# Performance work log

Measured on AMD Instinct MI355X. Metric: run time of the kernel, lower is better.

## Reference

```python
import jax, jax.numpy as jnp
import numpy as np

B, F, T, E, H = 32, 512, 2000, 256, 128
EPS = 1e-7


def setup_inputs() -> dict:
    key = jax.random.key(0)
    ks = jax.random.split(key, 12)
    s = 0.05
    return {
        "y1": jax.random.normal(ks[0], (B, F, T), jnp.float32),
        "in_state2": jnp.zeros((2, B, H, 2), jnp.float32),
        "enc_w": jax.random.normal(ks[1], (E, F), jnp.float32) * s,   # conv1x1 weight
        "gamma": jnp.ones((E,), jnp.float32),
        "beta": jnp.zeros((E,), jnp.float32),
        "Wih1": jax.random.normal(ks[2], (4 * H, E), jnp.float32) * s,
        "Whh1": jax.random.normal(ks[3], (4 * H, H), jnp.float32) * s,
        "bih1": jax.random.normal(ks[4], (4 * H,), jnp.float32) * s,
        "bhh1": jax.random.normal(ks[5], (4 * H,), jnp.float32) * s,
        "Wih2": jax.random.normal(ks[6], (4 * H, H), jnp.float32) * s,
        "Whh2": jax.random.normal(ks[7], (4 * H, H), jnp.float32) * s,
        "bih2": jax.random.normal(ks[8], (4 * H,), jnp.float32) * s,
        "bhh2": jax.random.normal(ks[9], (4 * H,), jnp.float32) * s,
        "Wd": jax.random.normal(ks[10], (E, H), jnp.float32) * s,    # dense: H -> E
        "bd": jnp.zeros((E,), jnp.float32),
        "dec_w": jax.random.normal(ks[11], (F, E), jnp.float32) * s, # conv1x1 weight
    }


def _lstm_scan(x_tbd, h0, c0, Wih, Whh, b):
    # x_tbd: [T, B, D]; torch gate order i, f, g, o
    def step(carry, xt):
        h, c = carry
        z = xt @ Wih.T + h @ Whh.T + b
        i, f, g, o = jnp.split(z, 4, axis=-1)
        c = jax.nn.sigmoid(f) * c + jax.nn.sigmoid(i) * jnp.tanh(g)
        h = jax.nn.sigmoid(o) * jnp.tanh(c)
        return (h, c), h
    (hT, cT), ys = jax.lax.scan(step, (h0, c0), x_tbd)
    return ys, hT, cT


def reference(y1, in_state2, enc_w, gamma, beta, Wih1, Whh1, bih1, bhh1,
              Wih2, Whh2, bih2, bhh2, Wd, bd, dec_w):
    # encoder conv1x1: [B, F, T] -> [B, T, E]
    enc = jnp.einsum('ef,bft->bte', enc_w, y1)
    # instant (channel-wise) layer norm over E
    mean = jnp.mean(enc, axis=-1, keepdims=True)
    var = jnp.mean(jnp.square(enc - mean), axis=-1, keepdims=True)
    normed = (enc - mean) / jnp.sqrt(var + EPS) * gamma + beta
    # separation block (dropout is identity in eval mode)
    h1, c1 = in_state2[0, :, :, 0], in_state2[0, :, :, 1]
    h2, c2 = in_state2[1, :, :, 0], in_state2[1, :, :, 1]
    x_tbd = jnp.transpose(normed, (1, 0, 2))          # [T, B, E]
    ys1, h1o, c1o = _lstm_scan(x_tbd, h1, c1, Wih1, Whh1, bih1 + bhh1)
    ys2, h2o, c2o = _lstm_scan(ys1, h2, c2, Wih2, Whh2, bih2 + bhh2)
    x2 = jnp.transpose(ys2, (1, 0, 2))                # [B, T, H]
    mask = jax.nn.sigmoid(x2 @ Wd.T + bd)             # [B, T, E]
    estimated = mask * enc                            # [B, T, E]
    decoded = jnp.einsum('fe,bte->bft', dec_w, estimated)  # [B, F, T]
    h = jnp.stack([h1o, h2o], axis=0)                 # [2, B, H]
    c = jnp.stack([c1o, c2o], axis=0)
    out_state = jnp.stack([h, c], axis=-1)            # [2, B, H, 2]
    return decoded, out_state
```

## Files before the change

kernel.cpp:

```cpp
#include <hip/hip_runtime.h>

typedef __bf16 bf16;
typedef __bf16 bf16x8 __attribute__((ext_vector_type(8)));
typedef float f32x4 __attribute__((ext_vector_type(4)));

#define MFMA16(a, b, c) __builtin_amdgcn_mfma_f32_16x16x32_bf16((a), (b), (c), 0, 0, 0)

static constexpr int Bn = 32, Fn = 512, Tn = 2000, En = 256, Hn = 128, G4 = 512;
static constexpr long DECN = 32768000;

__device__ __forceinline__ float sigm(float x) {
  float e = __builtin_amdgcn_exp2f(x * -1.442695040888963f);
  return __builtin_amdgcn_rcpf(1.0f + e);
}
__device__ __forceinline__ float tanh_(float x) {
  float e = __builtin_amdgcn_exp2f(x * 2.885390081777926f);
  return 1.0f - 2.0f * __builtin_amdgcn_rcpf(e + 1.0f);
}
__device__ __forceinline__ float b2f(ushort u) {
  union { float f; unsigned v; } x; x.v = ((unsigned)u) << 16; return x.f;
}
__device__ __forceinline__ ushort f2b(float f) {
  return __builtin_bit_cast(ushort, (bf16)f);
}

__global__ void k_detect(const unsigned* __restrict__ gamma_raw, int* __restrict__ flag) {
  if (threadIdx.x == 0) *flag = (gamma_raw[0] == 0x3F803F80u) ? 0 : 1;
}

struct CvtArgs {
  const void* src[15];
  long n[15];
  long off[15];
};
__global__ void k_cvt_all(CvtArgs args, bf16* __restrict__ prm,
                          const int* __restrict__ flag) {
  int seg = blockIdx.y;
  long n = args.n[seg];
  bf16* dst = prm + args.off[seg];
  long i = blockIdx.x * (long)blockDim.x + threadIdx.x;
  long stride = (long)gridDim.x * blockDim.x;
  if (*flag) {
    const float* s = (const float*)args.src[seg];
    for (; i < n; i += stride) dst[i] = (bf16)s[i];
  } else {
    const bf16* s = (const bf16*)args.src[seg];
    for (; i < n; i += stride) dst[i] = s[i];
  }
}

__global__ void k_transpose(const void* __restrict__ y1, bf16* __restrict__ y1T,
                            const int* __restrict__ flag) {
  __shared__ ushort tile[32][34];
  int tx = threadIdx.x, ty = threadIdx.y;
  int b = blockIdx.z, f0 = blockIdx.y * 32, t0 = blockIdx.x * 32;
  int isf32 = *flag;
  ushort* dst = (ushort*)y1T;
#pragma unroll
  for (int j = 0; j < 4; ++j) {
    int fl = ty + 8 * j, t = t0 + tx;
    if (t < Tn) {
      long idx = ((long)b * Fn + f0 + fl) * Tn + t;
      tile[fl][tx] = isf32 ? f2b(((const float*)y1)[idx]) : ((const ushort*)y1)[idx];
    }
  }
  __syncthreads();
#pragma unroll
  for (int j = 0; j < 4; ++j) {
    int tl = ty + 8 * j, t = t0 + tl;
    if (t < Tn) dst[((long)b * Tn + t) * Fn + f0 + tx] = tile[tx][tl];
  }
}

__global__ __launch_bounds__(256) void k_enc_ln(
    const bf16* __restrict__ y1T, const bf16* __restrict__ enc_w,
    bf16* __restrict__ enc_b, float2* __restrict__ stats) {
  __shared__ float zl[16][257];
  int tid = threadIdx.x;
  int wv = tid >> 6, lane = tid & 63, q = lane >> 4, l16 = lane & 15;
  long bt0 = (long)blockIdx.x * 16;
  f32x4 acc[4] = {};
  const bf16* Arow = y1T + (bt0 + l16) * Fn;
  for (int kt = 0; kt < 16; ++kt) {
    bf16x8 a = *(const bf16x8*)(Arow + kt * 32 + q * 8);
#pragma unroll
    for (int i = 0; i < 4; ++i) {
      int nt = wv * 4 + i;
      bf16x8 bfr = *(const bf16x8*)(enc_w + (nt * 16 + l16) * Fn + kt * 32 + q * 8);
      acc[i] = MFMA16(a, bfr, acc[i]);
    }
  }
#pragma unroll
  for (int i = 0; i < 4; ++i) {
    int col = (wv * 4 + i) * 16 + l16;
#pragma unroll
    for (int r = 0; r < 4; ++r) zl[q * 4 + r][col] = acc[i][r];
  }
  __syncthreads();
  {
    int row = tid >> 4, ii = tid & 15;
    float s = 0.f, ss = 0.f;
#pragma unroll
    for (int j = 0; j < 16; ++j) { float v = zl[row][ii + 16 * j]; s += v; ss += v * v; }
#pragma unroll
    for (int m = 1; m < 16; m <<= 1) { s += __shfl_xor(s, m, 64); ss += __shfl_xor(ss, m, 64); }
    if (ii == 0) {
      float mean = s * (1.0f / 256.0f);
      float var = ss * (1.0f / 256.0f) - mean * mean;
      stats[bt0 + row] = make_float2(mean, rsqrtf(var + 1e-7f));
    }
  }
#pragma unroll
  for (int r = 0; r < 16; ++r)
    enc_b[(bt0 + r) * En + tid] = (bf16)zl[r][tid];
}

__global__ __launch_bounds__(256) void k_pre1(
    const bf16* __restrict__ enc_b, const float2* __restrict__ stats,
    const bf16* __restrict__ gamma, const bf16* __restrict__ beta,
    const bf16* __restrict__ Wih1, const bf16* __restrict__ bih1,
    const bf16* __restrict__ bhh1, bf16* __restrict__ pre1r) {
  int tid = threadIdx.x, wv = tid >> 6, lane = tid & 63, q = lane >> 4, l16 = lane & 15;
  int t = blockIdx.x >> 1, wh = blockIdx.x & 1;
  int b = wh * 16 + l16;
  long row = (long)b * Tn + t;
  float2 st = stats[row];
  const bf16* Arow = enc_b + row * En;
  f32x4 acc[8] = {};
  float bsum[8];
#pragma unroll
  for (int i = 0; i < 8; ++i) {
    int nt = wv * 8 + i;
    int orig = (nt & 3) * 128 + (nt >> 2) * 16 + l16;
    bsum[i] = (float)bih1[orig] + (float)bhh1[orig];
  }
  for (int kt = 0; kt < 8; ++kt) {
    bf16x8 a = *(const bf16x8*)(Arow + kt * 32 + q * 8);
    bf16x8 g8 = *(const bf16x8*)(gamma + kt * 32 + q * 8);
    bf16x8 e8 = *(const bf16x8*)(beta + kt * 32 + q * 8);
    bf16x8 x;
#pragma unroll
    for (int j = 0; j < 8; ++j) {
      float rg = st.y * (float)g8[j];
      x[j] = (bf16)((float)a[j] * rg + ((float)e8[j] - st.x * rg));
    }
#pragma unroll
    for (int i = 0; i < 8; ++i) {
      int nt = wv * 8 + i;
      int orig = (nt & 3) * 128 + (nt >> 2) * 16 + l16;
      bf16x8 bfr = *(const bf16x8*)(Wih1 + orig * En + kt * 32 + q * 8);
      acc[i] = MFMA16(x, bfr, acc[i]);
    }
  }
  ushort* dst = (ushort*)pre1r;
#pragma unroll
  for (int hg = 0; hg < 2; ++hg) {
    int hid = (wv * 2 + hg) * 16 + l16;
#pragma unroll
    for (int r = 0; r < 4; ++r) {
      int B = wh * 16 + q * 4 + r;
      ushort4 pk;
      pk.x = f2b(acc[hg * 4 + 0][r] + bsum[hg * 4 + 0]);
      pk.y = f2b(acc[hg * 4 + 1][r] + bsum[hg * 4 + 1]);
      pk.z = f2b(acc[hg * 4 + 2][r] + bsum[hg * 4 + 2]);
      pk.w = f2b(acc[hg * 4 + 3][r] + bsum[hg * 4 + 3]);
      *(ushort4*)(dst + (((long)t * Bn + B) * Hn + hid) * 4) = pk;
    }
  }
}

__global__ __launch_bounds__(512, 2) void k_rec(
    const bf16* __restrict__ pre1r, const bf16* __restrict__ state_c,
    const bf16* __restrict__ Whh1, const bf16* __restrict__ Wih2,
    const bf16* __restrict__ Whh2, const bf16* __restrict__ bih2,
    const bf16* __restrict__ bhh2, bf16* __restrict__ ys2,
    void* __restrict__ out_base, const int* __restrict__ flag) {
  __shared__ __align__(16) bf16 h1buf[2][16 * 136];
  __shared__ __align__(16) bf16 h2buf[2][16 * 136];

  int tid = threadIdx.x, wv = tid >> 6, lane = tid & 63, q = lane >> 4, l16 = lane & 15;
  int b0 = blockIdx.x * 4;
  int isf32 = *flag;
  int hid = wv * 16 + l16;
  int brow = b0 + q;
  int pos = q * 4;

  bf16x8 W1[4][4], Wx[4][4], Wh[4][4];
  float b2s[4];
#pragma unroll
  for (int g = 0; g < 4; ++g) {
    int n = g * 128 + hid;
#pragma unroll
    for (int kt = 0; kt < 4; ++kt) {
      W1[g][kt] = *(const bf16x8*)(Whh1 + n * Hn + kt * 32 + q * 8);
      Wx[g][kt] = *(const bf16x8*)(Wih2 + n * Hn + kt * 32 + q * 8);
      Wh[g][kt] = *(const bf16x8*)(Whh2 + n * Hn + kt * 32 + q * 8);
    }
    b2s[g] = (float)bih2[n] + (float)bhh2[n];
  }
#pragma unroll
  for (int g = 0; g < 4; ++g)
#pragma unroll
    for (int kt = 0; kt < 4; ++kt) {
      f32x4 t1 = __builtin_bit_cast(f32x4, W1[g][kt]);
      f32x4 t2 = __builtin_bit_cast(f32x4, Wx[g][kt]);
      f32x4 t3 = __builtin_bit_cast(f32x4, Wh[g][kt]);
      asm volatile("" : "+v"(t1), "+v"(t2), "+v"(t3));
      W1[g][kt] = __builtin_bit_cast(bf16x8, t1);
      Wx[g][kt] = __builtin_bit_cast(bf16x8, t2);
      Wh[g][kt] = __builtin_bit_cast(bf16x8, t3);
    }

  for (int i = tid; i < 16 * 136; i += 512) {
    h1buf[0][i] = (bf16)0.f; h1buf[1][i] = (bf16)0.f;
    h2buf[0][i] = (bf16)0.f; h2buf[1][i] = (bf16)0.f;
  }
  __syncthreads();

  float c1, c2;
  {
    long i1 = ((long)(0 * Bn + brow) * Hn + hid) * 2;
    long i2 = ((long)(1 * Bn + brow) * Hn + hid) * 2;
    h1buf[1][pos * 136 + hid] = state_c[i1];
    h2buf[1][pos * 136 + hid] = state_c[i2];
    c1 = (float)state_c[i1 + 1];
    c2 = (float)state_c[i2 + 1];
  }
  ushort4 pz = *(const ushort4*)((const ushort*)pre1r + ((long)brow * Hn + hid) * 4);
  __syncthreads();

  for (int t = 0; t < Tn; ++t) {
    int cur = t & 1, prv = cur ^ 1;
    f32x4 acc[4];
#pragma unroll
    for (int g = 0; g < 4; ++g) { f32x4 z = {}; acc[g] = z; }
    acc[0][0] = b2f(pz.x); acc[1][0] = b2f(pz.y);
    acc[2][0] = b2f(pz.z); acc[3][0] = b2f(pz.w);
    {
      int tn = (t + 1 < Tn) ? t + 1 : t;
      pz = *(const ushort4*)((const ushort*)pre1r +
                             (((long)tn * Bn + brow) * Hn + hid) * 4);
    }
#pragma unroll
    for (int kt = 0; kt < 4; ++kt) {
      bf16x8 a = *(const bf16x8*)(&h1buf[prv][l16 * 136 + kt * 32 + q * 8]);
#pragma unroll
      for (int g = 0; g < 4; ++g) acc[g] = MFMA16(a, W1[g][kt], acc[g]);
    }
    {
      float ig = sigm(acc[0][0]), fg = sigm(acc[1][0]);
      float gg = tanh_(acc[2][0]), og = sigm(acc[3][0]);
      c1 = fg * c1 + ig * gg;
      float h = og * tanh_(c1);
      h1buf[cur][pos * 136 + hid] = (bf16)h;
      if (t == Tn - 1) {
        long o = DECN + ((long)(0 * Bn + brow) * Hn + hid) * 2;
        if (isf32) { ((float*)out_base)[o] = h; ((float*)out_base)[o + 1] = c1; }
        else { ((bf16*)out_base)[o] = (bf16)h; ((bf16*)out_base)[o + 1] = (bf16)c1; }
      }
    }
    __syncthreads();
#pragma unroll
    for (int g = 0; g < 4; ++g) { f32x4 z = {}; acc[g] = z; acc[g][0] = b2s[g]; }
#pragma unroll
    for (int kt = 0; kt < 4; ++kt) {
      bf16x8 ax = *(const bf16x8*)(&h1buf[cur][l16 * 136 + kt * 32 + q * 8]);
      bf16x8 ah = *(const bf16x8*)(&h2buf[prv][l16 * 136 + kt * 32 + q * 8]);
#pragma unroll
      for (int g = 0; g < 4; ++g) {
        acc[g] = MFMA16(ax, Wx[g][kt], acc[g]);
        acc[g] = MFMA16(ah, Wh[g][kt], acc[g]);
      }
    }
    {
      float ig = sigm(acc[0][0]), fg = sigm(acc[1][0]);
      float gg = tanh_(acc[2][0]), og = sigm(acc[3][0]);
      c2 = fg * c2 + ig * gg;
      float h = og * tanh_(c2);
      h2buf[cur][pos * 136 + hid] = (bf16)h;
      ys2[((long)brow * Tn + t) * Hn + hid] = (bf16)h;
      if (t == Tn - 1) {
        long o = DECN + ((long)(1 * Bn + brow) * Hn + hid) * 2;
        if (isf32) { ((float*)out_base)[o] = h; ((float*)out_base)[o + 1] = c2; }
        else { ((bf16*)out_base)[o] = (bf16)h; ((bf16*)out_base)[o + 1] = (bf16)c2; }
      }
    }
    __syncthreads();
  }
}

__global__ __launch_bounds__(256) void k_mask(
    const bf16* __restrict__ ys2, const bf16* __restrict__ Wd,
    const bf16* __restrict__ bd, bf16* __restrict__ enc_est) {
  int tid = threadIdx.x, wv = tid >> 6, lane = tid & 63, q = lane >> 4, l16 = lane & 15;
  long bt0 = (long)blockIdx.x * 16;
  f32x4 acc[4] = {};
  const bf16* Arow = ys2 + (bt0 + l16) * Hn;
  for (int kt = 0; kt < 4; ++kt) {
    bf16x8 a = *(const bf16x8*)(Arow + kt * 32 + q * 8);
#pragma unroll
    for (int i = 0; i < 4; ++i) {
      int nt = wv * 4 + i;
      bf16x8 bfr = *(const bf16x8*)(Wd + (nt * 16 + l16) * Hn + kt * 32 + q * 8);
      acc[i] = MFMA16(a, bfr, acc[i]);
    }
  }
#pragma unroll
  for (int i = 0; i < 4; ++i) {
    int col = (wv * 4 + i) * 16 + l16;
    float bdv = (float)bd[col];
#pragma unroll
    for (int r = 0; r < 4; ++r) {
      int row = q * 4 + r;
      float m = sigm(acc[i][r] + bdv);
      long idx = (bt0 + row) * En + col;
      enc_est[idx] = (bf16)(m * (float)enc_est[idx]);
    }
  }
}

__global__ __launch_bounds__(256) void k_dec(
    const bf16* __restrict__ est_b, const bf16* __restrict__ dec_w,
    void* __restrict__ outp, const int* __restrict__ flag) {
  int tid = threadIdx.x, wv = tid >> 6, lane = tid & 63, q = lane >> 4, l16 = lane & 15;
  long bt0 = (long)blockIdx.x * 16;
  int b = (int)(bt0 / Tn), t0 = (int)(bt0 % Tn);
  int isf32 = *flag;
  f32x4 acc[8] = {};
  const bf16* Arow = est_b + (bt0 + l16) * En;
  for (int kt = 0; kt < 8; ++kt) {
    bf16x8 a = *(const bf16x8*)(Arow + kt * 32 + q * 8);
#pragma unroll
    for (int i = 0; i < 8; ++i) {
      int nt = wv * 8 + i;
      bf16x8 bfr = *(const bf16x8*)(dec_w + (nt * 16 + l16) * En + kt * 32 + q * 8);
      acc[i] = MFMA16(a, bfr, acc[i]);
    }
  }
#pragma unroll
  for (int i = 0; i < 8; ++i) {
    int f = (wv * 8 + i) * 16 + l16;
    long off = ((long)b * Fn + f) * Tn + t0 + q * 4;
    if (isf32) {
      *(float4*)((float*)outp + off) =
          make_float4(acc[i][0], acc[i][1], acc[i][2], acc[i][3]);
    } else {
      ushort4 pk;
      pk.x = f2b(acc[i][0]);
      pk.y = f2b(acc[i][1]);
      pk.z = f2b(acc[i][2]);
      pk.w = f2b(acc[i][3]);
      *(ushort4*)((ushort*)outp + off) = pk;
    }
  }
}

extern "C" void kernel_launch(void* const* d_in, const int* in_sizes, int n_in,
                              void* d_out, int out_size, void* d_ws, size_t ws_size,
                              hipStream_t stream) {
  (void)in_sizes; (void)n_in; (void)out_size; (void)ws_size;

  char* ws = (char*)d_ws;
  bf16*   enc_b = (bf16*)(ws);
  float2* stats = (float2*)(ws + 32768000);
  bf16*   ys2   = (bf16*)(ws + 33280000);
  bf16*   prm   = (bf16*)(ws + 49664000);
  int*    flag  = (int*)(ws + 50947584);

  static const long pn[15] = {131072, 256, 256, 131072, 65536, 512, 512,
                              65536, 65536, 512, 512, 32768, 256, 131072, 16384};
  static const int  src_idx[15] = {2, 3, 4, 5, 6, 7, 8, 9, 10, 11, 12, 13, 14, 15, 1};
  long poff[15]; long o = 0;
  for (int i = 0; i < 15; ++i) { poff[i] = o; o += pn[i]; }
  bf16* enc_w = prm + poff[0];
  bf16* gamma = prm + poff[1];
  bf16* beta  = prm + poff[2];
  bf16* Wih1  = prm + poff[3];
  bf16* Whh1  = prm + poff[4];
  bf16* bih1  = prm + poff[5];
  bf16* bhh1  = prm + poff[6];
  bf16* Wih2  = prm + poff[7];
  bf16* Whh2  = prm + poff[8];
  bf16* bih2  = prm + poff[9];
  bf16* bhh2  = prm + poff[10];
  bf16* Wd    = prm + poff[11];
  bf16* bd    = prm + poff[12];
  bf16* dec_w = prm + poff[13];
  bf16* state_c = prm + poff[14];

  bf16* y1T   = (bf16*)d_out;
  bf16* pre1r = (bf16*)d_out;

  k_detect<<<1, 64, 0, stream>>>((const unsigned*)d_in[3], flag);
  CvtArgs ca;
  for (int i = 0; i < 15; ++i) {
    ca.src[i] = d_in[src_idx[i]];
    ca.n[i] = pn[i];
    ca.off[i] = poff[i];
  }
  k_cvt_all<<<dim3(512, 15, 1), 256, 0, stream>>>(ca, prm, flag);
  k_transpose<<<dim3(63, 16, 32), dim3(32, 8, 1), 0, stream>>>(d_in[0], y1T, flag);
  k_enc_ln<<<4000, 256, 0, stream>>>(y1T, enc_w, enc_b, stats);
  k_pre1<<<4000, 256, 0, stream>>>(enc_b, stats, gamma, beta, Wih1, bih1, bhh1, pre1r);
  k_rec<<<8, 512, 0, stream>>>(pre1r, state_c, Whh1, Wih2, Whh2, bih2, bhh2,
                               ys2, d_out, flag);
  k_mask<<<4000, 256, 0, stream>>>(ys2, Wd, bd, enc_b);
  k_dec<<<4000, 256, 0, stream>>>(enc_b, dec_w, d_out, flag);
}
```

Before: 3.002 ms.

## Compact LSTM hidden-state LDS layout and use lightweight LDS-only barriers

```diff
diff --git a/kernel.cpp b/kernel.cpp
--- a/kernel.cpp
+++ b/kernel.cpp
@@ -5,6 +5,7 @@
 typedef float f32x4 __attribute__((ext_vector_type(4)));
 
 #define MFMA16(a, b, c) __builtin_amdgcn_mfma_f32_16x16x32_bf16((a), (b), (c), 0, 0, 0)
+#define LBAR() asm volatile("s_waitcnt lgkmcnt(0)\n\ts_barrier" ::: "memory")
 
 static constexpr int Bn = 32, Fn = 512, Tn = 2000, En = 256, Hn = 128, G4 = 512;
 static constexpr long DECN = 32768000;
@@ -175,18 +176,17 @@
     const bf16* __restrict__ Whh2, const bf16* __restrict__ bih2,
     const bf16* __restrict__ bhh2, bf16* __restrict__ ys2,
     void* __restrict__ out_base, const int* __restrict__ flag) {
-  __shared__ __align__(16) bf16 h1buf[2][16 * 136];
-  __shared__ __align__(16) bf16 h2buf[2][16 * 136];
+  __shared__ __align__(16) char h1s[2 * 1088];
+  __shared__ __align__(16) char h2s[2 * 1088];
 
   int tid = threadIdx.x, wv = tid >> 6, lane = tid & 63, q = lane >> 4, l16 = lane & 15;
   int b0 = blockIdx.x * 4;
   int isf32 = *flag;
   int hid = wv * 16 + l16;
   int brow = b0 + q;
-  int pos = q * 4;
 
   bf16x8 W1[4][4], Wx[4][4], Wh[4][4];
-  float b2s[4];
+  unsigned b2lo, b2hi;
 #pragma unroll
   for (int g = 0; g < 4; ++g) {
     int n = g * 128 + hid;
@@ -196,7 +196,16 @@
       Wx[g][kt] = *(const bf16x8*)(Wih2 + n * Hn + kt * 32 + q * 8);
       Wh[g][kt] = *(const bf16x8*)(Whh2 + n * Hn + kt * 32 + q * 8);
     }
-    b2s[g] = (float)bih2[n] + (float)bhh2[n];
+  }
+  {
+    ushort u[4];
+#pragma unroll
+    for (int g = 0; g < 4; ++g) {
+      int n = g * 128 + hid;
+      u[g] = f2b((float)bih2[n] + (float)bhh2[n]);
+    }
+    b2lo = (unsigned)u[0] | ((unsigned)u[1] << 16);
+    b2hi = (unsigned)u[2] | ((unsigned)u[3] << 16);
   }
 #pragma unroll
   for (int g = 0; g < 4; ++g)
@@ -211,81 +220,97 @@
       Wh[g][kt] = __builtin_bit_cast(bf16x8, t3);
     }
 
-  for (int i = tid; i < 16 * 136; i += 512) {
-    h1buf[0][i] = (bf16)0.f; h1buf[1][i] = (bf16)0.f;
-    h2buf[0][i] = (bf16)0.f; h2buf[1][i] = (bf16)0.f;
+  if (tid < 272) {
+    ((int*)h1s)[tid] = 0; ((int*)h1s)[tid + 272] = 0;
+    ((int*)h2s)[tid] = 0; ((int*)h2s)[tid + 272] = 0;
   }
   __syncthreads();
+
+  int wb = (hid >> 5) * 272 + ((hid >> 3) & 3) * 64 + q * 16 + (hid & 7) * 2;
+  int rbase = ((l16 & 3) == 0) ? (q * 64 + (l16 >> 2) * 16) : 256;
 
   float c1, c2;
   {
-    long i1 = ((long)(0 * Bn + brow) * Hn + hid) * 2;
-    long i2 = ((long)(1 * Bn + brow) * Hn + hid) * 2;
-    h1buf[1][pos * 136 + hid] = state_c[i1];
-    h2buf[1][pos * 136 + hid] = state_c[i2];
+    long i1 = ((long)brow * Hn + hid) * 2;
+    long i2 = ((long)(Bn + brow) * Hn + hid) * 2;
+    *(bf16*)(h1s + wb) = state_c[i1];
+    *(bf16*)(h2s + 1088 + wb) = state_c[i2];
     c1 = (float)state_c[i1 + 1];
     c2 = (float)state_c[i2 + 1];
   }
-  ushort4 pz = *(const ushort4*)((const ushort*)pre1r + ((long)brow * Hn + hid) * 4);
-  __syncthreads();
+  LBAR();
+  bf16x8 ax[4], ah[4];
+#pragma unroll
+  for (int kt = 0; kt < 4; ++kt)
+    ax[kt] = *(const bf16x8*)(h1s + rbase + kt * 272);
+  LBAR();
+
+  const ushort* pzp = (const ushort*)pre1r + ((long)brow * Hn + hid) * 4;
+  bf16* yp = ys2 + (long)brow * Tn * Hn + hid;
+  ushort4 pz = *(const ushort4*)pzp;
 
   for (int t = 0; t < Tn; ++t) {
-    int cur = t & 1, prv = cur ^ 1;
+    int o1c = (t & 1) * 1088;
+    int o2p = 1088 - o1c;
+    int tn = (t + 1 < Tn) ? t + 1 : t;
+    ushort4 pzn = *(const ushort4*)(pzp + (long)tn * (Bn * Hn * 4));
+#pragma unroll
+    for (int kt = 0; kt < 4; ++kt)
+      ah[kt] = *(const bf16x8*)(h2s + o2p + rbase + kt * 272);
+
     f32x4 acc[4];
-#pragma unroll
-    for (int g = 0; g < 4; ++g) { f32x4 z = {}; acc[g] = z; }
-    acc[0][0] = b2f(pz.x); acc[1][0] = b2f(pz.y);
-    acc[2][0] = b2f(pz.z); acc[3][0] = b2f(pz.w);
-    {
-      int tn = (t + 1 < Tn) ? t + 1 : t;
-      pz = *(const ushort4*)((const ushort*)pre1r +
-                             (((long)tn * Bn + brow) * Hn + hid) * 4);
-    }
-#pragma unroll
-    for (int kt = 0; kt < 4; ++kt) {
-      bf16x8 a = *(const bf16x8*)(&h1buf[prv][l16 * 136 + kt * 32 + q * 8]);
-#pragma unroll
-      for (int g = 0; g < 4; ++g) acc[g] = MFMA16(a, W1[g][kt], acc[g]);
-    }
+    acc[0] = (f32x4){b2f(pz.x), 0.f, 0.f, 0.f};
+    acc[1] = (f32x4){b2f(pz.y), 0.f, 0.f, 0.f};
+    acc[2] = (f32x4){b2f(pz.z), 0.f, 0.f, 0.f};
+    acc[3] = (f32x4){b2f(pz.w), 0.f, 0.f, 0.f};
+#pragma unroll
+    for (int kt = 0; kt < 4; ++kt)
+#pragma unroll
+      for (int g = 0; g < 4; ++g) acc[g] = MFMA16(ax[kt], W1[g][kt], acc[g]);
     {
       float ig = sigm(acc[0][0]), fg = sigm(acc[1][0]);
       float gg = tanh_(acc[2][0]), og = sigm(acc[3][0]);
       c1 = fg * c1 + ig * gg;
       float h = og * tanh_(c1);
-      h1buf[cur][pos * 136 + hid] = (bf16)h;
+      *(bf16*)(h1s + o1c + wb) = (bf16)h;
       if (t == Tn - 1) {
-        long o = DECN + ((long)(0 * Bn + brow) * Hn + hid) * 2;
+        long o = DECN + ((long)brow * Hn + hid) * 2;
         if (isf32) { ((float*)out_base)[o] = h; ((float*)out_base)[o + 1] = c1; }
         else { ((bf16*)out_base)[o] = (bf16)h; ((bf16*)out_base)[o + 1] = (bf16)c1; }
       }
     }
-    __syncthreads();
-#pragma unroll
-    for (int g = 0; g < 4; ++g) { f32x4 z = {}; acc[g] = z; acc[g][0] = b2s[g]; }
-#pragma unroll
-    for (int kt = 0; kt < 4; ++kt) {
-      bf16x8 ax = *(const bf16x8*)(&h1buf[cur][l16 * 136 + kt * 32 + q * 8]);
-      bf16x8 ah = *(const bf16x8*)(&h2buf[prv][l16 * 136 + kt * 32 + q * 8]);
-#pragma unroll
-      for (int g = 0; g < 4; ++g) {
-        acc[g] = MFMA16(ax, Wx[g][kt], acc[g]);
-        acc[g] = MFMA16(ah, Wh[g][kt], acc[g]);
-      }
-    }
+    LBAR();
+
+#pragma unroll
+    for (int kt = 0; kt < 4; ++kt)
+      ax[kt] = *(const bf16x8*)(h1s + o1c + rbase + kt * 272);
+    acc[0] = (f32x4){b2f((ushort)(b2lo & 0xffffu)), 0.f, 0.f, 0.f};
+    acc[1] = (f32x4){b2f((ushort)(b2lo >> 16)), 0.f, 0.f, 0.f};
+    acc[2] = (f32x4){b2f((ushort)(b2hi & 0xffffu)), 0.f, 0.f, 0.f};
+    acc[3] = (f32x4){b2f((ushort)(b2hi >> 16)), 0.f, 0.f, 0.f};
+#pragma unroll
+    for (int kt = 0; kt < 4; ++kt)
+#pragma unroll
+      for (int g = 0; g < 4; ++g) acc[g] = MFMA16(ah[kt], Wh[g][kt], acc[g]);
+#pragma unroll
+    for (int kt = 0; kt < 4; ++kt)
+#pragma unroll
+      for (int g = 0; g < 4; ++g) acc[g] = MFMA16(ax[kt], Wx[g][kt], acc[g]);
     {
       float ig = sigm(acc[0][0]), fg = sigm(acc[1][0]);
       float gg = tanh_(acc[2][0]), og = sigm(acc[3][0]);
       c2 = fg * c2 + ig * gg;
       float h = og * tanh_(c2);
-      h2buf[cur][pos * 136 + hid] = (bf16)h;
-      ys2[((long)brow * Tn + t) * Hn + hid] = (bf16)h;
+      *(bf16*)(h2s + o1c + wb) = (bf16)h;
+      yp[(long)t * Hn] = (bf16)h;
       if (t == Tn - 1) {
-        long o = DECN + ((long)(1 * Bn + brow) * Hn + hid) * 2;
+        long o = DECN + ((long)(Bn + brow) * Hn + hid) * 2;
         if (isf32) { ((float*)out_base)[o] = h; ((float*)out_base)[o + 1] = c2; }
         else { ((bf16*)out_base)[o] = (bf16)h; ((bf16*)out_base)[o + 1] = (bf16)c2; }
       }
     }
-    __syncthreads();
+    pz = pzn;
+    LBAR();
   }
 }
 
```

After: 3.791 ms. +26.3%, slower.
